# Kernel tuning notes

Measured on AMD Instinct MI355X. Metric: run time of the kernel, lower is better.

The kernel has to match this reference:

```python
import jax, jax.numpy as jnp
import numpy as np

B, OBS, H, OUT, T = 4096, 256, 1024, 256, 20


def setup_inputs() -> dict:
    key = jax.random.key(0)
    ks = jax.random.split(key, 10)
    def w(k, shape, fan_in, scale=1.0):
        return (jax.random.normal(k, shape, jnp.float32) / np.sqrt(fan_in)) * scale
    return {
        "x": jax.random.normal(ks[0], (B, OBS), jnp.float32),
        "h": jax.random.normal(ks[1], (B, H), jnp.float32) * 0.1,
        "c": jax.random.normal(ks[2], (B, H), jnp.float32) * 0.1,
        "t": jnp.arange(T, dtype=jnp.float32) * 0.05,  # sorted time grid, total span ~1
        "W_i2h": w(ks[3], (OBS + H, H), OBS + H),
        "b_i2h": jnp.zeros((H,), jnp.float32),
        "W_h2o": w(ks[4], (H, OUT), H),
        "b_h2o": jnp.zeros((OUT,), jnp.float32),
        "Wf1": w(ks[5], (H, H), H),
        "bf1": jnp.zeros((H,), jnp.float32),
        "Wf2": w(ks[6], (H, H), H, scale=0.1),  # keep ODE dynamics mild
        "bf2": jnp.zeros((H,), jnp.float32),
    }


def _odeint_rk4(f, h0, t):
    # Fixed-step RK4 through the given time grid; returns solution at t[-1]
    dts = jnp.diff(t)
    def step(h, dt):
        k1 = f(h)
        k2 = f(h + 0.5 * dt * k1)
        k3 = f(h + 0.5 * dt * k2)
        k4 = f(h + dt * k3)
        return h + (dt / 6.0) * (k1 + 2.0 * k2 + 2.0 * k3 + k4), None
    hT, _ = jax.lax.scan(step, h0, dts)
    return hT


def reference(x, h, c, t, W_i2h, b_i2h, W_h2o, b_h2o, Wf1, bf1, Wf2, bf2):
    # ODE RHS: Linear -> tanh -> Linear (autonomous)
    func = lambda hh: jnp.tanh(hh @ Wf1 + bf1) @ Wf2 + bf2
    # i, f, o gates are identical in the original (same Linear on same 'combined'):
    gate = jax.nn.sigmoid(jnp.concatenate([x, h], axis=-1) @ W_i2h + b_i2h)
    h_ode = _odeint_rk4(func, h, t)
    c_tilde = jax.nn.sigmoid(jnp.concatenate([x, h_ode], axis=-1) @ W_i2h + b_i2h)
    c_new = gate * c + gate * c_tilde  # f*c + i*c_tilde with f == i == gate
    h_new = gate * jnp.tanh(c_new)     # o == gate
    out = h_new @ W_h2o + b_h2o
    return out, h_new, c_new
```

## Files before the change

kernel.cpp:

```cpp
#include <hip/hip_runtime.h>
#include <stdint.h>
#include <math.h>


typedef __attribute__((ext_vector_type(8))) short short8;
typedef __attribute__((ext_vector_type(4))) float float4v;

#define BK 64

__device__ __forceinline__ float bf2f(unsigned short u) {
  union { unsigned int i; float f; } x;
  x.i = ((unsigned int)u) << 16;
  return x.f;
}
__device__ __forceinline__ unsigned short f2bf(float f) {
  union { float f; unsigned int i; } x;
  x.f = f;
  unsigned int r = x.i + 0x7fffu + ((x.i >> 16) & 1u);
  return (unsigned short)(r >> 16);
}
__device__ __forceinline__ void load16(const void* g, void* l) {
  __builtin_amdgcn_global_load_lds(
      (__attribute__((address_space(1))) void*)g,
      (__attribute__((address_space(3))) void*)l, 16, 0, 0);
}
__device__ __forceinline__ short8 packbf8(const float* p) {
  float4v lo = *(const float4v*)p, hi = *(const float4v*)(p + 4);
  short8 s;
  s[0] = (short)f2bf(lo[0]); s[1] = (short)f2bf(lo[1]);
  s[2] = (short)f2bf(lo[2]); s[3] = (short)f2bf(lo[3]);
  s[4] = (short)f2bf(hi[0]); s[5] = (short)f2bf(hi[1]);
  s[6] = (short)f2bf(hi[2]); s[7] = (short)f2bf(hi[3]);
  return s;
}
__device__ __forceinline__ short8 pack2(float4v lo, float4v hi) {
  short8 s;
  s[0] = (short)f2bf(lo[0]); s[1] = (short)f2bf(lo[1]);
  s[2] = (short)f2bf(lo[2]); s[3] = (short)f2bf(lo[3]);
  s[4] = (short)f2bf(hi[0]); s[5] = (short)f2bf(hi[1]);
  s[6] = (short)f2bf(hi[2]); s[7] = (short)f2bf(hi[3]);
  return s;
}
__device__ __forceinline__ float vsub_uniform(float a, float b) {
  float av;
  asm("v_mov_b32 %0, %1" : "=v"(av) : "s"(a));
  return av - b;
}

template <int MODE, int ADT>
__global__ __launch_bounds__(256, 4) void gemm_ode(
    const void* Av, const unsigned short* __restrict__ Bt,
    int N, int K,
    const float* __restrict__ bias, const float* __restrict__ tgrid,
    int step, int first,
    unsigned short* __restrict__ u1b,
    unsigned short* __restrict__ Tb,
    unsigned short* __restrict__ Sb,
    unsigned short* __restrict__ t1dst,
    const void* aux,
    const float* __restrict__ c2,
    float* __restrict__ outF) {
  __shared__ short8 AsV[2][512];
  __shared__ short8 BsV[2][512];

  const int t = threadIdx.x;
  int bx = blockIdx.x, by = blockIdx.y;
  if (gridDim.x == 16 && gridDim.y == 64) {
    const int lin = bx + (by << 4);
    const int x = lin & 7, j = lin >> 3;
    bx = j & 15;
    by = (x << 3) | (j >> 4);
  }
  const int mBase = by * 64, nBase = bx * 64;
  const int wave = t >> 6, lane = t & 63;
  const int wr = wave >> 1, wc = wave & 1;
  const int q = lane >> 4, m16 = lane & 15;

  float4v acc[2][2];
#pragma unroll
  for (int r = 0; r < 2; ++r)
#pragma unroll
    for (int c = 0; c < 2; ++c) acc[r][c] = (float4v){0.f, 0.f, 0.f, 0.f};

  const int r0 = t >> 3;
  const int kcl = (t & 7) ^ (r0 & 7);
  const unsigned short* aU = (const unsigned short*)Av + (size_t)(mBase + r0) * K + kcl * 8;
  const float* aF = (const float*)Av + (size_t)(mBase + r0) * K + kcl * 8;
  const unsigned short* bG = Bt + (size_t)(nBase + r0) * K + kcl * 8;

  auto computeT = [&](int buf) {
#pragma unroll
    for (int kk = 0; kk < 2; ++kk) {
      const int kc = kk * 4 + q;
      short8 af[2], bfr[2];
#pragma unroll
      for (int r = 0; r < 2; ++r) {
        const int arow = wr * 32 + r * 16 + m16;
        af[r] = AsV[buf][arow * 8 + (kc ^ (arow & 7))];
        const int brow = wc * 32 + r * 16 + m16;
        bfr[r] = BsV[buf][brow * 8 + (kc ^ (brow & 7))];
      }
#pragma unroll
      for (int r = 0; r < 2; ++r)
#pragma unroll
        for (int c = 0; c < 2; ++c)
          acc[r][c] = __builtin_amdgcn_mfma_f32_16x16x32_bf16(af[r], bfr[c],
                                                              acc[r][c], 0, 0, 0);
    }
  };

  if constexpr (ADT == 1) {
    auto stageT = [&](int buf, int k0) {
      load16(aU + k0, &AsV[buf][t]);
      load16(aU + (size_t)32 * K + k0, &AsV[buf][t + 256]);
      load16(bG + k0, &BsV[buf][t]);
      load16(bG + (size_t)32 * K + k0, &BsV[buf][t + 256]);
    };
    stageT(0, 0);
    int cur = 0;
    for (int k0 = BK; k0 < K; k0 += BK) {
      stageT(cur ^ 1, k0);
      asm volatile("s_waitcnt vmcnt(4)" ::: "memory");
      __builtin_amdgcn_sched_barrier(0);
      __builtin_amdgcn_s_barrier();
      __builtin_amdgcn_sched_barrier(0);
      computeT(cur);
      asm volatile("s_waitcnt lgkmcnt(0)" ::: "memory");
      __builtin_amdgcn_sched_barrier(0);
      __builtin_amdgcn_s_barrier();
      __builtin_amdgcn_sched_barrier(0);
      cur ^= 1;
    }
    asm volatile("s_waitcnt vmcnt(0)" ::: "memory");
    __builtin_amdgcn_sched_barrier(0);
    __builtin_amdgcn_s_barrier();
    __builtin_amdgcn_sched_barrier(0);
    computeT(cur);
  } else {
    for (int k0 = 0; k0 < K; k0 += BK) {
      AsV[0][t] = packbf8(aF + k0);
      AsV[0][t + 256] = packbf8(aF + (size_t)32 * K + k0);
      load16(bG + k0, &BsV[0][t]);
      load16(bG + (size_t)32 * K + k0, &BsV[0][t + 256]);
      __builtin_amdgcn_s_waitcnt(0);
      __syncthreads();
      computeT(0);
      __syncthreads();
    }
  }

  float dtv = 0.f;
  if constexpr (MODE >= 1 && MODE <= 4) dtv = vsub_uniform(tgrid[step + 1], tgrid[step]);
  if constexpr (MODE == 5) dtv = vsub_uniform(tgrid[step], tgrid[0]);

  const int colBase = nBase + wc * 32 + m16;
  const int rowBase = mBase + wr * 32 + q * 4;
#pragma unroll
  for (int r = 0; r < 2; ++r) {
#pragma unroll
    for (int c = 0; c < 2; ++c) {
      const int col = colBase + c * 16;
#pragma unroll
      for (int e = 0; e < 4; ++e) {
        const int row = rowBase + r * 16 + e;
        const size_t idx = (size_t)row * N + col;
        const float v = acc[r][c][e];
        if constexpr (MODE == 0) {
          const float u1 = v + bias[col];
          u1b[idx] = f2bf(u1);
          t1dst[idx] = f2bf(tanhf(u1));
        } else if constexpr (MODE == 1) {
          const float u2 = bf2f(u1b[idx]) + 0.5f * dtv * (v + c2[col]);
          const float th = tanhf(u2);
          t1dst[idx] = f2bf(th);
          Tb[idx] = f2bf(bf2f(((const unsigned short*)aux)[idx]) + 2.f * th);
        } else if constexpr (MODE == 2) {
          const float u3 = bf2f(u1b[idx]) + 0.5f * dtv * (v + c2[col]);
          const float th = tanhf(u3);
          t1dst[idx] = f2bf(th);
          Tb[idx] = f2bf(bf2f(Tb[idx]) + 2.f * th);
        } else if constexpr (MODE == 3) {
          const float u4 = bf2f(u1b[idx]) + dtv * (v + c2[col]);
          Tb[idx] = f2bf(bf2f(Tb[idx]) + tanhf(u4));
        } else if constexpr (MODE == 4) {
          const float u1n = bf2f(u1b[idx]) + (dtv * (1.f / 6.f)) * v + dtv * c2[col];
          u1b[idx] = f2bf(u1n);
          t1dst[idx] = f2bf(tanhf(u1n));
          const float sOld = first ? 0.f : bf2f(Sb[idx]);
          Sb[idx] = f2bf(sOld + (dtv * (1.f / 6.f)) *
                                    bf2f(((const unsigned short*)aux)[idx]));
        } else if constexpr (MODE == 5) {
          const float z = ((const float*)aux)[idx] + v + dtv * bias[col];
          t1dst[idx] = f2bf(z);
        } else if constexpr (MODE == 6) {
          t1dst[(size_t)col * 1024 + row] = f2bf(v);
        } else {
          outF[idx] = v + bias[col];
        }
      }
    }
  }
}

__global__ __launch_bounds__(256, 4) void gemm_fused(
    const float* __restrict__ x, const float* __restrict__ h,
    const unsigned short* __restrict__ zB,
    const unsigned short* __restrict__ WiT,
    const float* __restrict__ bi, const float* __restrict__ c_in,
    float* __restrict__ hnewF, float* __restrict__ cnewF) {
  __shared__ short8 AsG[512];
  __shared__ short8 AsC[512];
  __shared__ short8 Bs[2][512];

  const int t = threadIdx.x;
  int bx = blockIdx.x, by = blockIdx.y;
  {
    const int lin = bx + (by << 4);
    const int xc = lin & 7, j = lin >> 3;
    bx = j & 15;
    by = (xc << 3) | (j >> 4);
  }
  const int mBase = by * 64, nBase = bx * 64;
  const int wave = t >> 6, lane = t & 63;
  const int wr = wave >> 1, wc = wave & 1;
  const int q = lane >> 4, m16 = lane & 15;

  float4v accG[2][2], accC[2][2];
#pragma unroll
  for (int r = 0; r < 2; ++r)
#pragma unroll
    for (int c = 0; c < 2; ++c) {
      accG[r][c] = (float4v){0.f, 0.f, 0.f, 0.f};
      accC[r][c] = (float4v){0.f, 0.f, 0.f, 0.f};
    }

  const int r0 = t >> 3;
  const int kcl = (t & 7) ^ (r0 & 7);
  const int row0 = mBase + r0, row1 = row0 + 32;

  struct Regs { float4v a0, a1, a2, a3; short8 z0, z1; };
  Regs Ra, Rb;

  auto issueA = [&](int i, Regs& R) {
    const int k0 = i * 64;
    if (k0 < 256) {
      const float* g0 = x + (size_t)row0 * 256 + k0 + kcl * 8;
      const float* g1 = x + (size_t)row1 * 256 + k0 + kcl * 8;
      R.a0 = *(const float4v*)g0; R.a1 = *(const float4v*)(g0 + 4);
      R.a2 = *(const float4v*)g1; R.a3 = *(const float4v*)(g1 + 4);
      R.z0 = *(const short8*)(const void*)g0;
      R.z1 = *(const short8*)(const void*)g1;
    } else {
      const size_t o0 = (size_t)row0 * 1024 + (k0 - 256) + kcl * 8;
      const size_t o1 = (size_t)row1 * 1024 + (k0 - 256) + kcl * 8;
      R.a0 = *(const float4v*)(h + o0); R.a1 = *(const float4v*)(h + o0 + 4);
      R.a2 = *(const float4v*)(h + o1); R.a3 = *(const float4v*)(h + o1 + 4);
      R.z0 = *(const short8*)(zB + o0);
      R.z1 = *(const short8*)(zB + o1);
    }
  };
  auto issueB = [&](int i, int buf) {
    const int k0 = i * 64;
    load16(WiT + (size_t)(nBase + r0) * 1280 + k0 + kcl * 8, &Bs[buf][t]);
    load16(WiT + (size_t)(nBase + r0 + 32) * 1280 + k0 + kcl * 8,
           &Bs[buf][t + 256]);
  };
  auto computeF = [&](int buf) {
#pragma unroll
    for (int kk = 0; kk < 2; ++kk) {
      const int kc = kk * 4 + q;
      short8 ag[2], ac[2], bfr[2];
#pragma unroll
      for (int r = 0; r < 2; ++r) {
        const int arow = wr * 32 + r * 16 + m16;
        ag[r] = AsG[arow * 8 + (kc ^ (arow & 7))];
        ac[r] = AsC[arow * 8 + (kc ^ (arow & 7))];
        const int brow = wc * 32 + r * 16 + m16;
        bfr[r] = Bs[buf][brow * 8 + (kc ^ (brow & 7))];
      }
#pragma unroll
      for (int r = 0; r < 2; ++r)
#pragma unroll
        for (int c = 0; c < 2; ++c) {
          accG[r][c] = __builtin_amdgcn_mfma_f32_16x16x32_bf16(ag[r], bfr[c],
                                                               accG[r][c], 0, 0, 0);
          accC[r][c] = __builtin_amdgcn_mfma_f32_16x16x32_bf16(ac[r], bfr[c],
                                                               accC[r][c], 0, 0, 0);
        }
    }
  };

  int buf = 0;
  auto stepF = [&](int i, Regs& Rc, Regs& Rn) {
    if (i + 1 < 20) {
      issueA(i + 1, Rn);
      issueB(i + 1, buf ^ 1);
      asm volatile("s_waitcnt vmcnt(8)" ::: "memory");
    } else {
      asm volatile("s_waitcnt vmcnt(0)" ::: "memory");
    }
    __builtin_amdgcn_sched_barrier(0);
    {
      const bool isX = (i * 64) < 256;
      const short8 s0 = pack2(Rc.a0, Rc.a1);
      const short8 s1 = pack2(Rc.a2, Rc.a3);
      AsG[t] = s0;
      AsG[t + 256] = s1;
      AsC[t] = isX ? s0 : Rc.z0;
      AsC[t + 256] = isX ? s1 : Rc.z1;
    }
    asm volatile("s_waitcnt lgkmcnt(0)" ::: "memory");
    __builtin_amdgcn_sched_barrier(0);
    __builtin_amdgcn_s_barrier();
    __builtin_amdgcn_sched_barrier(0);
    computeF(buf);
    asm volatile("s_waitcnt lgkmcnt(0)" ::: "memory");
    __builtin_amdgcn_sched_barrier(0);
    __builtin_amdgcn_s_barrier();
    __builtin_amdgcn_sched_barrier(0);
    buf ^= 1;
  };

  issueA(0, Ra);
  issueB(0, 0);
#pragma unroll 1
  for (int ii = 0; ii < 20; ii += 2) {
    stepF(ii, Ra, Rb);
    stepF(ii + 1, Rb, Ra);
  }

  const int colBase = nBase + wc * 32 + m16;
  const int rowBase = mBase + wr * 32 + q * 4;
#pragma unroll
  for (int r = 0; r < 2; ++r) {
#pragma unroll
    for (int c = 0; c < 2; ++c) {
      const int col = colBase + c * 16;
      const float bv = bi[col];
#pragma unroll
      for (int e = 0; e < 4; ++e) {
        const int row = rowBase + r * 16 + e;
        const size_t idx = (size_t)row * 1024 + col;
        const float g = 1.f / (1.f + expf(-(accG[r][c][e] + bv)));
        const float ct = 1.f / (1.f + expf(-(accC[r][c][e] + bv)));
        const float cn = g * (c_in[idx] + ct);
        const float hn = g * tanhf(cn);
        hnewF[idx] = hn;
        cnewF[idx] = cn;
      }
    }
  }
}

__global__ __launch_bounds__(256) void transpose_f32_bf16(
    const float* __restrict__ in, unsigned short* __restrict__ out,
    int R, int C) {
  __shared__ float tile[32][33];
  const int c0 = blockIdx.x * 32, r0 = blockIdx.y * 32;
  const int tx = threadIdx.x, ty = threadIdx.y;
#pragma unroll
  for (int i = 0; i < 32; i += 8)
    tile[ty + i][tx] = in[(size_t)(r0 + ty + i) * C + c0 + tx];
  __syncthreads();
#pragma unroll
  for (int i = 0; i < 32; i += 8)
    out[(size_t)(c0 + ty + i) * R + r0 + tx] = f2bf(tile[tx][ty + i]);
}

__global__ __launch_bounds__(256) void c2_gemv(
    const float* __restrict__ b2, const float* __restrict__ W1,
    float* __restrict__ c2v) {
  const int n = blockIdx.x * 256 + threadIdx.x;
  float a = 0.f;
  for (int k = 0; k < 1024; ++k) a += b2[k] * W1[(size_t)k * 1024 + n];
  c2v[n] = a;
}

extern "C" void kernel_launch(void* const* d_in, const int* in_sizes, int n_in,
                              void* d_out, int out_size, void* d_ws, size_t ws_size,
                              hipStream_t stream) {
  const float* x  = (const float*)d_in[0];
  const float* h  = (const float*)d_in[1];
  const float* c  = (const float*)d_in[2];
  const float* t  = (const float*)d_in[3];
  const float* Wi = (const float*)d_in[4];
  const float* bi = (const float*)d_in[5];
  const float* Wo = (const float*)d_in[6];
  const float* bo = (const float*)d_in[7];
  const float* W1 = (const float*)d_in[8];
  const float* b1 = (const float*)d_in[9];
  const float* W2 = (const float*)d_in[10];
  const float* b2 = (const float*)d_in[11];

  const size_t MB = 1ull << 20;
  char* ws = (char*)d_ws;
  unsigned short* W21T = (unsigned short*)(ws);
  unsigned short* W2T  = (unsigned short*)(ws + 2 * MB);
  unsigned short* WiT  = (unsigned short*)(ws + 4 * MB);
  unsigned short* WoT  = (unsigned short*)(ws + 6 * MB + 512 * 1024);
  unsigned short* P0   = (unsigned short*)(ws + 7 * MB);

  float*          outF  = (float*)d_out;
  float*          hnewF = outF + 1048576;
  float*          cnewF = outF + 5242880;
  unsigned short* u1b   = (unsigned short*)d_out;
  unsigned short* Tb    = (unsigned short*)((char*)d_out + 8 * MB);
  unsigned short* P1    = (unsigned short*)((char*)d_out + 16 * MB);
  unsigned short* Sb    = (unsigned short*)((char*)d_out + 24 * MB);
  unsigned short* W1T   = (unsigned short*)((char*)d_out + 32 * MB);
  float*          c2v   = (float*)((char*)d_out + 34 * MB);

  const dim3 tb(32, 8), blk(256), g(16, 64);

  transpose_f32_bf16<<<dim3(32, 32), tb, 0, stream>>>(W1, W1T, 1024, 1024);
  transpose_f32_bf16<<<dim3(32, 32), tb, 0, stream>>>(W2, W2T, 1024, 1024);
  transpose_f32_bf16<<<dim3(32, 40), tb, 0, stream>>>(Wi, WiT, 1280, 1024);
  transpose_f32_bf16<<<dim3(8, 32),  tb, 0, stream>>>(Wo, WoT, 1024, 256);
  c2_gemv<<<4, blk, 0, stream>>>(b2, W1, c2v);
  gemm_ode<6, 0><<<dim3(16, 16), blk, 0, stream>>>(
      W2, W1T, 1024, 1024, b1, t, 0, 0,
      nullptr, nullptr, nullptr, W21T, nullptr, nullptr, nullptr);
  gemm_ode<0, 0><<<g, blk, 0, stream>>>(
      h, W1T, 1024, 1024, b1, t, 0, 0,
      u1b, nullptr, nullptr, P0, nullptr, nullptr, nullptr);

  for (int s = 0; s < 19; ++s) {
    gemm_ode<1, 1><<<g, blk, 0, stream>>>(
        P0, W21T, 1024, 1024, b1, t, s, 0,
        u1b, Tb, nullptr, P1, P0, c2v, nullptr);
    gemm_ode<2, 1><<<g, blk, 0, stream>>>(
        P1, W21T, 1024, 1024, b1, t, s, 0,
        u1b, Tb, nullptr, P0, nullptr, c2v, nullptr);
    gemm_ode<3, 1><<<g, blk, 0, stream>>>(
        P0, W21T, 1024, 1024, b1, t, s, 0,
        u1b, Tb, nullptr, nullptr, nullptr, c2v, nullptr);
    gemm_ode<4, 1><<<g, blk, 0, stream>>>(
        Tb, W21T, 1024, 1024, b1, t, s, (s == 0) ? 1 : 0,
        u1b, nullptr, Sb, P0, Tb, c2v, nullptr);
  }

  gemm_ode<5, 1><<<g, blk, 0, stream>>>(
      Sb, W2T, 1024, 1024, b2, t, 19, 0,
      nullptr, nullptr, nullptr, P0, h, nullptr, nullptr);

  gemm_fused<<<g, blk, 0, stream>>>(x, h, P0, WiT, bi, c, hnewF, cnewF);

  gemm_ode<7, 0><<<dim3(4, 64), blk, 0, stream>>>(
      hnewF, WoT, 256, 1024, bo, t, 0, 0,
      nullptr, nullptr, nullptr, nullptr, nullptr, nullptr, outF);
}
```

Before: 1.730 ms.

## Prefetch epilogue operands during last K tile and pipeline fp32 A loads

```diff
diff --git a/kernel.cpp b/kernel.cpp
--- a/kernel.cpp
+++ b/kernel.cpp
@@ -23,15 +23,6 @@
   __builtin_amdgcn_global_load_lds(
       (__attribute__((address_space(1))) void*)g,
       (__attribute__((address_space(3))) void*)l, 16, 0, 0);
-}
-__device__ __forceinline__ short8 packbf8(const float* p) {
-  float4v lo = *(const float4v*)p, hi = *(const float4v*)(p + 4);
-  short8 s;
-  s[0] = (short)f2bf(lo[0]); s[1] = (short)f2bf(lo[1]);
-  s[2] = (short)f2bf(lo[2]); s[3] = (short)f2bf(lo[3]);
-  s[4] = (short)f2bf(hi[0]); s[5] = (short)f2bf(hi[1]);
-  s[6] = (short)f2bf(hi[2]); s[7] = (short)f2bf(hi[3]);
-  return s;
 }
 __device__ __forceinline__ short8 pack2(float4v lo, float4v hi) {
   short8 s;
@@ -88,7 +79,10 @@
   const float* aF = (const float*)Av + (size_t)(mBase + r0) * K + kcl * 8;
   const unsigned short* bG = Bt + (size_t)(nBase + r0) * K + kcl * 8;
 
-  auto computeT = [&](int buf) {
+  const int colBase = nBase + wc * 32 + m16;
+  const int rowBase = mBase + wr * 32 + q * 4;
+
+  auto computeT = [&](int bufA, int bufB) {
 #pragma unroll
     for (int kk = 0; kk < 2; ++kk) {
       const int kc = kk * 4 + q;
@@ -96,9 +90,9 @@
 #pragma unroll
       for (int r = 0; r < 2; ++r) {
         const int arow = wr * 32 + r * 16 + m16;
-        af[r] = AsV[buf][arow * 8 + (kc ^ (arow & 7))];
+        af[r] = AsV[bufA][arow * 8 + (kc ^ (arow & 7))];
         const int brow = wc * 32 + r * 16 + m16;
-        bfr[r] = BsV[buf][brow * 8 + (kc ^ (brow & 7))];
+        bfr[r] = BsV[bufB][brow * 8 + (kc ^ (brow & 7))];
       }
 #pragma unroll
       for (int r = 0; r < 2; ++r)
@@ -108,6 +102,12 @@
                                                               acc[r][c], 0, 0, 0);
     }
   };
+
+  unsigned short preA[2][2][4];
+  unsigned short preB[2][2][4];
+  unsigned short preC[2][2][4];
+  float preF[2][2][4];
+  float c2pre[2];
 
   if constexpr (ADT == 1) {
     auto stageT = [&](int buf, int k0) {
@@ -118,34 +118,107 @@
     };
     stageT(0, 0);
     int cur = 0;
-    for (int k0 = BK; k0 < K; k0 += BK) {
+#pragma unroll 1
+    for (int k0 = BK; k0 < K - BK; k0 += BK) {
       stageT(cur ^ 1, k0);
       asm volatile("s_waitcnt vmcnt(4)" ::: "memory");
       __builtin_amdgcn_sched_barrier(0);
       __builtin_amdgcn_s_barrier();
       __builtin_amdgcn_sched_barrier(0);
-      computeT(cur);
+      computeT(cur, cur);
       asm volatile("s_waitcnt lgkmcnt(0)" ::: "memory");
       __builtin_amdgcn_sched_barrier(0);
       __builtin_amdgcn_s_barrier();
       __builtin_amdgcn_sched_barrier(0);
       cur ^= 1;
     }
+    stageT(cur ^ 1, K - BK);
+    {
+#pragma unroll
+      for (int r = 0; r < 2; ++r)
+#pragma unroll
+        for (int c = 0; c < 2; ++c) {
+          const int col = colBase + c * 16;
+#pragma unroll
+          for (int e = 0; e < 4; ++e) {
+            const int row = rowBase + r * 16 + e;
+            const size_t idx = (size_t)row * N + col;
+            if constexpr (MODE >= 1 && MODE <= 4) preA[r][c][e] = u1b[idx];
+            if constexpr (MODE == 1 || MODE == 4)
+              preB[r][c][e] = ((const unsigned short*)aux)[idx];
+            if constexpr (MODE == 2 || MODE == 3) preB[r][c][e] = Tb[idx];
+            if constexpr (MODE == 4) preC[r][c][e] = Sb[idx];
+            if constexpr (MODE == 5) preF[r][c][e] = ((const float*)aux)[idx];
+          }
+        }
+#pragma unroll
+      for (int c = 0; c < 2; ++c) {
+        if constexpr (MODE >= 1 && MODE <= 4) c2pre[c] = c2[colBase + c * 16];
+        if constexpr (MODE == 5) c2pre[c] = bias[colBase + c * 16];
+      }
+    }
+    if constexpr (MODE == 4)
+      asm volatile("s_waitcnt vmcnt(54)" ::: "memory");
+    else if constexpr (MODE == 5)
+      asm volatile("s_waitcnt vmcnt(22)" ::: "memory");
+    else
+      asm volatile("s_waitcnt vmcnt(38)" ::: "memory");
+    __builtin_amdgcn_sched_barrier(0);
+    __builtin_amdgcn_s_barrier();
+    __builtin_amdgcn_sched_barrier(0);
+    computeT(cur, cur);
+    asm volatile("s_waitcnt lgkmcnt(0)" ::: "memory");
+    __builtin_amdgcn_sched_barrier(0);
+    __builtin_amdgcn_s_barrier();
+    __builtin_amdgcn_sched_barrier(0);
+    cur ^= 1;
     asm volatile("s_waitcnt vmcnt(0)" ::: "memory");
     __builtin_amdgcn_sched_barrier(0);
     __builtin_amdgcn_s_barrier();
     __builtin_amdgcn_sched_barrier(0);
-    computeT(cur);
+    computeT(cur, cur);
   } else {
-    for (int k0 = 0; k0 < K; k0 += BK) {
-      AsV[0][t] = packbf8(aF + k0);
-      AsV[0][t + 256] = packbf8(aF + (size_t)32 * K + k0);
-      load16(bG + k0, &BsV[0][t]);
-      load16(bG + (size_t)32 * K + k0, &BsV[0][t + 256]);
-      __builtin_amdgcn_s_waitcnt(0);
-      __syncthreads();
-      computeT(0);
-      __syncthreads();
+    struct RegsF { float4v a0, a1, a2, a3; };
+    RegsF Ra, Rb;
+    auto issueAF = [&](int k0, RegsF& R) {
+      R.a0 = *(const float4v*)(aF + k0);
+      R.a1 = *(const float4v*)(aF + k0 + 4);
+      R.a2 = *(const float4v*)(aF + (size_t)32 * K + k0);
+      R.a3 = *(const float4v*)(aF + (size_t)32 * K + k0 + 4);
+    };
+    auto issueBF = [&](int buf, int k0) {
+      load16(bG + k0, &BsV[buf][t]);
+      load16(bG + (size_t)32 * K + k0, &BsV[buf][t + 256]);
+    };
+    issueAF(0, Ra);
+    issueBF(0, 0);
+    int bufB = 0;
+    auto stepI = [&](int k0, RegsF& Rc, RegsF& Rn) {
+      if (k0 + BK < K) {
+        issueAF(k0 + BK, Rn);
+        issueBF(bufB ^ 1, k0 + BK);
+        asm volatile("s_waitcnt vmcnt(6)" ::: "memory");
+      } else {
+        asm volatile("s_waitcnt vmcnt(0)" ::: "memory");
+      }
+      __builtin_amdgcn_sched_barrier(0);
+      AsV[0][t] = pack2(Rc.a0, Rc.a1);
+      AsV[0][t + 256] = pack2(Rc.a2, Rc.a3);
+      asm volatile("s_waitcnt lgkmcnt(0)" ::: "memory");
+      __builtin_amdgcn_sched_barrier(0);
+      __builtin_amdgcn_s_barrier();
+      __builtin_amdgcn_sched_barrier(0);
+      computeT(0, bufB);
+      asm volatile("s_waitcnt lgkmcnt(0)" ::: "memory");
+      __builtin_amdgcn_sched_barrier(0);
+      __builtin_amdgcn_s_barrier();
+      __builtin_amdgcn_sched_barrier(0);
+      bufB ^= 1;
+    };
+#pragma unroll 1
+    for (int k0 = 0; k0 < K; k0 += 2 * BK) {
+      stepI(k0, Ra, Rb);
+      stepI(k0 + BK, Rb, Ra);
     }
   }
 
@@ -153,8 +226,6 @@
   if constexpr (MODE >= 1 && MODE <= 4) dtv = vsub_uniform(tgrid[step + 1], tgrid[step]);
   if constexpr (MODE == 5) dtv = vsub_uniform(tgrid[step], tgrid[0]);
 
-  const int colBase = nBase + wc * 32 + m16;
-  const int rowBase = mBase + wr * 32 + q * 4;
 #pragma unroll
   for (int r = 0; r < 2; ++r) {
 #pragma unroll
@@ -170,27 +241,26 @@
           u1b[idx] = f2bf(u1);
           t1dst[idx] = f2bf(tanhf(u1));
         } else if constexpr (MODE == 1) {
-          const float u2 = bf2f(u1b[idx]) + 0.5f * dtv * (v + c2[col]);
+          const float u2 = bf2f(preA[r][c][e]) + 0.5f * dtv * (v + c2pre[c]);
           const float th = tanhf(u2);
           t1dst[idx] = f2bf(th);
-          Tb[idx] = f2bf(bf2f(((const unsigned short*)aux)[idx]) + 2.f * th);
+          Tb[idx] = f2bf(bf2f(preB[r][c][e]) + 2.f * th);
         } else if constexpr (MODE == 2) {
-          const float u3 = bf2f(u1b[idx]) + 0.5f * dtv * (v + c2[col]);
+          const float u3 = bf2f(preA[r][c][e]) + 0.5f * dtv * (v + c2pre[c]);
           const float th = tanhf(u3);
           t1dst[idx] = f2bf(th);
-          Tb[idx] = f2bf(bf2f(Tb[idx]) + 2.f * th);
+          Tb[idx] = f2bf(bf2f(preB[r][c][e]) + 2.f * th);
         } else if constexpr (MODE == 3) {
-          const float u4 = bf2f(u1b[idx]) + dtv * (v + c2[col]);
-          Tb[idx] = f2bf(bf2f(Tb[idx]) + tanhf(u4));
+          const float u4 = bf2f(preA[r][c][e]) + dtv * (v + c2pre[c]);
+          Tb[idx] = f2bf(bf2f(preB[r][c][e]) + tanhf(u4));
         } else if constexpr (MODE == 4) {
-          const float u1n = bf2f(u1b[idx]) + (dtv * (1.f / 6.f)) * v + dtv * c2[col];
+          const float u1n = bf2f(preA[r][c][e]) + (dtv * (1.f / 6.f)) * v + dtv * c2pre[c];
           u1b[idx] = f2bf(u1n);
           t1dst[idx] = f2bf(tanhf(u1n));
-          const float sOld = first ? 0.f : bf2f(Sb[idx]);
-          Sb[idx] = f2bf(sOld + (dtv * (1.f / 6.f)) *
-                                    bf2f(((const unsigned short*)aux)[idx]));
+          const float sOld = first ? 0.f : bf2f(preC[r][c][e]);
+          Sb[idx] = f2bf(sOld + (dtv * (1.f / 6.f)) * bf2f(preB[r][c][e]));
         } else if constexpr (MODE == 5) {
-          const float z = ((const float*)aux)[idx] + v + dtv * bias[col];
+          const float z = preF[r][c][e] + v + dtv * c2pre[c];
           t1dst[idx] = f2bf(z);
         } else if constexpr (MODE == 6) {
           t1dst[(size_t)col * 1024 + row] = f2bf(v);
@@ -352,28 +422,55 @@
   }
 }
 
-__global__ __launch_bounds__(256) void transpose_f32_bf16(
-    const float* __restrict__ in, unsigned short* __restrict__ out,
-    int R, int C) {
-  __shared__ float tile[32][33];
-  const int c0 = blockIdx.x * 32, r0 = blockIdx.y * 32;
-  const int tx = threadIdx.x, ty = threadIdx.y;
-#pragma unroll
-  for (int i = 0; i < 32; i += 8)
-    tile[ty + i][tx] = in[(size_t)(r0 + ty + i) * C + c0 + tx];
-  __syncthreads();
-#pragma unroll
-  for (int i = 0; i < 32; i += 8)
-    out[(size_t)(c0 + ty + i) * R + r0 + tx] = f2bf(tile[tx][ty + i]);
-}
-
-__global__ __launch_bounds__(256) void c2_gemv(
-    const float* __restrict__ b2, const float* __restrict__ W1,
+__global__ __launch_bounds__(256) void prep_all(
+    const float* __restrict__ W1, const float* __restrict__ W2,
+    const float* __restrict__ Wi, const float* __restrict__ Wo,
+    const float* __restrict__ b2,
+    unsigned short* __restrict__ W1T, unsigned short* __restrict__ W2T,
+    unsigned short* __restrict__ WiT, unsigned short* __restrict__ WoT,
     float* __restrict__ c2v) {
-  const int n = blockIdx.x * 256 + threadIdx.x;
-  float a = 0.f;
-  for (int k = 0; k < 1024; ++k) a += b2[k] * W1[(size_t)k * 1024 + n];
-  c2v[n] = a;
+  const int bid = blockIdx.x;
+  const int t = threadIdx.x;
+  if (bid < 3584) {
+    const float* in;
+    unsigned short* out;
+    int R, C, bx, by;
+    if (bid < 1024) {
+      in = W1; out = W1T; R = 1024; C = 1024;
+      bx = bid & 31; by = bid >> 5;
+    } else if (bid < 2048) {
+      in = W2; out = W2T; R = 1024; C = 1024;
+      const int b = bid - 1024; bx = b & 31; by = b >> 5;
+    } else if (bid < 3328) {
+      in = Wi; out = WiT; R = 1280; C = 1024;
+      const int b = bid - 2048; bx = b & 31; by = b >> 5;
+    } else {
+      in = Wo; out = WoT; R = 1024; C = 256;
+      const int b = bid - 3328; bx = b & 7; by = b >> 3;
+    }
+    __shared__ float tile[32][33];
+    const int c0 = bx * 32, r0 = by * 32;
+    const int tx = t & 31, ty = t >> 5;
+#pragma unroll
+    for (int i = 0; i < 32; i += 8)
+      tile[ty + i][tx] = in[(size_t)(r0 + ty + i) * C + c0 + tx];
+    __syncthreads();
+#pragma unroll
+    for (int i = 0; i < 32; i += 8)
+      out[(size_t)(c0 + ty + i) * R + r0 + tx] = f2bf(tile[tx][ty + i]);
+  } else {
+    __shared__ float part[4][64];
+    const int b = bid - 3584;
+    const int nl = t & 63, kq = t >> 6;
+    const int n = b * 64 + nl;
+    float a = 0.f;
+    for (int k = kq * 256; k < kq * 256 + 256; ++k)
+      a += b2[k] * W1[(size_t)k * 1024 + n];
+    part[kq][nl] = a;
+    __syncthreads();
+    if (kq == 0)
+      c2v[n] = ((part[0][nl] + part[1][nl]) + part[2][nl]) + part[3][nl];
+  }
 }
 
 extern "C" void kernel_launch(void* const* d_in, const int* in_sizes, int n_in,
@@ -410,13 +507,10 @@
   unsigned short* W1T   = (unsigned short*)((char*)d_out + 32 * MB);
   float*          c2v   = (float*)((char*)d_out + 34 * MB);
 
-  const dim3 tb(32, 8), blk(256), g(16, 64);
-
-  transpose_f32_bf16<<<dim3(32, 32), tb, 0, stream>>>(W1, W1T, 1024, 1024);
-  transpose_f32_bf16<<<dim3(32, 32), tb, 0, stream>>>(W2, W2T, 1024, 1024);
-  transpose_f32_bf16<<<dim3(32, 40), tb, 0, stream>>>(Wi, WiT, 1280, 1024);
-  transpose_f32_bf16<<<dim3(8, 32),  tb, 0, stream>>>(Wo, WoT, 1024, 256);
-  c2_gemv<<<4, blk, 0, stream>>>(b2, W1, c2v);
+  const dim3 blk(256), g(16, 64);
+
+  prep_all<<<3600, blk, 0, stream>>>(W1, W2, Wi, Wo, b2,
+                                     W1T, W2T, WiT, WoT, c2v);
   gemm_ode<6, 0><<<dim3(16, 16), blk, 0, stream>>>(
       W2, W1T, 1024, 1024, b1, t, 0, 0,
       nullptr, nullptr, nullptr, W21T, nullptr, nullptr, nullptr);
```

New measurement: 1.647 ms. -4.8%, faster.
